# Kernel optimization log

Measured on AMD Instinct MI355X. Metric: run time of the kernel, lower is better.

Reference implementation:

```python
import jax, jax.numpy as jnp
import numpy as np
import math

B, T, C, H = 4, 2048, 1024, 4
D = C // H
SCALE = 1.0 / math.sqrt(D)
EPS = 1e-5

def _cln(x, w, b):
    # channel-first LayerNorm over C of (B, C, T)
    mu = jnp.mean(x, axis=1, keepdims=True)
    r = x - mu
    s = jnp.mean(r * r, axis=1, keepdims=True)
    return r / jnp.sqrt(s + EPS) * w + b

def _dwconv(x, w, b=None):
    # depthwise conv1d: x (B, C, T), w (C, 1, 3), stride 1, pad 1
    y = jax.lax.conv_general_dilated(x, w, (1,), [(1, 1)], dimension_numbers=('NCH', 'OIH', 'NCH'), feature_group_count=x.shape[1])
    if b is not None:
        y = y + b[None, :, None]
    return y

def _conv1x1(x, w, b):
    # pointwise conv: x (B, C, T), w (Cout, Cin), b (Cout,)
    return jnp.einsum('oc,bct->bot', w, x) + b[None, :, None]

def _forward(x, mask, norm1_w, norm1_b, qconv_w, kconv_w, vconv_w, qnorm_w, qnorm_b, knorm_w, knorm_b, vnorm_w, vnorm_b, q1_w, q1_b, k1_w, k1_b, v1_w, v1_b, proj_w, proj_b, norm2_w, norm2_b, lin1_w, lin1_b, tc_w, tc_b, lin2_w, lin2_b):
    xc = jnp.swapaxes(x, 1, 2)                      # (B, C, T)
    h = _cln(xc, norm1_w, norm1_b)
    mf = mask.astype(x.dtype)                       # (B, 1, T); stride 1 -> interpolate is identity
    q = _conv1x1(_cln(_dwconv(h, qconv_w) * mf, qnorm_w, qnorm_b), q1_w, q1_b)
    k = _conv1x1(_cln(_dwconv(h, kconv_w) * mf, knorm_w, knorm_b), k1_w, k1_b)
    v = _conv1x1(_cln(_dwconv(h, vconv_w) * mf, vnorm_w, vnorm_b), v1_w, v1_b)
    # (B, H, T, D)
    q = jnp.swapaxes(q.reshape(B, H, D, T), 2, 3)
    k = jnp.swapaxes(k.reshape(B, H, D, T), 2, 3)
    v = jnp.swapaxes(v.reshape(B, H, D, T), 2, 3)
    att = jnp.einsum('bhqd,bhkd->bhqk', q * SCALE, k)
    att = jnp.where(mask[:, :, None, :], att, -jnp.inf)
    att = jax.nn.softmax(att, axis=-1)
    out = jnp.einsum('bhqk,bhkd->bhqd', att, v * mf[:, :, :, None])
    out = jnp.swapaxes(out, 2, 3).reshape(B, C, T)
    out = _conv1x1(out, proj_w, proj_b) * mf        # qx_mask == mask for stride 1
    x = x + jnp.swapaxes(out, 1, 2)                 # residual, (B, T, C)
    # Local_cnn branch
    h2 = jnp.swapaxes(_cln(jnp.swapaxes(x, 1, 2), norm2_w, norm2_b), 1, 2)  # (B, T, C)
    y = h2 @ lin1_w.T + lin1_b
    y = jnp.swapaxes(_dwconv(jnp.swapaxes(y, 1, 2), tc_w, tc_b), 1, 2)
    y = jax.nn.gelu(y, approximate=False)
    y = y @ lin2_w.T + lin2_b
    return x + y

def setup_inputs():
    key = jax.random.key(0)
    ks = jax.random.split(key, 16)
    f32 = jnp.float32
    x = jax.random.normal(ks[0], (B, T, C), dtype=f32)
    lengths = jax.random.randint(ks[1], (B,), T // 2, T + 1)
    mask = jnp.arange(T)[None, None, :] < lengths[:, None, None]  # (B, 1, T) bool
    dw_std = math.sqrt(2.0 / 3.0)
    px_std = math.sqrt(2.0 / C)
    d = dict(x=x, mask=mask)
    d['norm1_w'] = jnp.ones((1, C, 1), f32); d['norm1_b'] = jnp.zeros((1, C, 1), f32)
    d['qconv_w'] = jax.random.normal(ks[2], (C, 1, 3), dtype=f32) * dw_std
    d['kconv_w'] = jax.random.normal(ks[3], (C, 1, 3), dtype=f32) * dw_std
    d['vconv_w'] = jax.random.normal(ks[4], (C, 1, 3), dtype=f32) * dw_std
    for nm in ['qnorm', 'knorm', 'vnorm']:
        d[nm + '_w'] = jnp.ones((1, C, 1), f32); d[nm + '_b'] = jnp.zeros((1, C, 1), f32)
    d['q1_w'] = jax.random.normal(ks[5], (C, C), dtype=f32) * px_std; d['q1_b'] = jnp.zeros((C,), f32)
    d['k1_w'] = jax.random.normal(ks[6], (C, C), dtype=f32) * px_std; d['k1_b'] = jnp.zeros((C,), f32)
    d['v1_w'] = jax.random.normal(ks[7], (C, C), dtype=f32) * px_std; d['v1_b'] = jnp.zeros((C,), f32)
    d['proj_w'] = jax.random.normal(ks[8], (C, C), dtype=f32) * px_std; d['proj_b'] = jnp.zeros((C,), f32)
    d['norm2_w'] = jnp.ones((1, C, 1), f32); d['norm2_b'] = jnp.zeros((1, C, 1), f32)
    d['lin1_w'] = jax.random.normal(ks[9], (C, C), dtype=f32) * 0.02; d['lin1_b'] = jnp.zeros((C,), f32)
    d['tc_w'] = jax.random.normal(ks[10], (C, 1, 3), dtype=f32) * dw_std; d['tc_b'] = jnp.zeros((C,), f32)
    d['lin2_w'] = jax.random.normal(ks[11], (C, C), dtype=f32) * 0.02; d['lin2_b'] = jnp.zeros((C,), f32)
    return d

def reference(x, mask, norm1_w, norm1_b, qconv_w, kconv_w, vconv_w, qnorm_w, qnorm_b, knorm_w, knorm_b, vnorm_w, vnorm_b, q1_w, q1_b, k1_w, k1_b, v1_w, v1_b, proj_w, proj_b, norm2_w, norm2_b, lin1_w, lin1_b, tc_w, tc_b, lin2_w, lin2_b):
    return _forward(x, mask, norm1_w, norm1_b, qconv_w, kconv_w, vconv_w, qnorm_w, qnorm_b, knorm_w, knorm_b, vnorm_w, vnorm_b, q1_w, q1_b, k1_w, k1_b, v1_w, v1_b, proj_w, proj_b, norm2_w, norm2_b, lin1_w, lin1_b, tc_w, tc_b, lin2_w, lin2_b)
```

## Files before the change

kernel.cpp:

```cpp
#include <hip/hip_runtime.h>

#define BB 4
#define TT 2048
#define CC 1024
#define HH 4
#define DD 256
#define MM (BB*TT)

#define EPSV 1e-5f
#define NEGBIG (-1e30f)
#define SCALEV 0.0625f

typedef unsigned short u16;
typedef unsigned int   u32;
typedef __bf16 bf16x8 __attribute__((ext_vector_type(8)));
typedef float  f32x4  __attribute__((ext_vector_type(4)));

typedef u32 __attribute__((address_space(1))) gu32;
typedef u32 __attribute__((address_space(3))) lu32;

__device__ __forceinline__ u16 f2bf(float f){
  u32 u = __builtin_bit_cast(u32, f);
  u32 r = (u + 0x7fffu + ((u >> 16) & 1u)) >> 16;
  return (u16)r;
}
__device__ __forceinline__ float bf2f(u16 h){
  u32 u = ((u32)h) << 16;
  return __builtin_bit_cast(float, u);
}
__device__ __forceinline__ void gload_lds16(const u16* g, u16* l){
  __builtin_amdgcn_global_load_lds((const gu32*)g, (lu32*)l, 16, 0, 0);
}
__device__ __forceinline__ u32 cvtpk_bf16(float lo, float hi){
  u32 r;
  asm("v_cvt_pk_bf16_f32 %0, %1, %2" : "=v"(r) : "v"(lo), "v"(hi));
  return r;
}

__global__ __launch_bounds__(256) void conv_w_kernel(
    const float* __restrict__ w0, const float* __restrict__ w1, const float* __restrict__ w2,
    const float* __restrict__ w3, const float* __restrict__ w4, const float* __restrict__ w5,
    u16* __restrict__ o0, u16* __restrict__ o1, u16* __restrict__ o2,
    u16* __restrict__ o3, u16* __restrict__ o4, u16* __restrict__ o5){
  const int i = (blockIdx.x * 256 + threadIdx.x) * 4;
  const float* wsrc[6] = {w0,w1,w2,w3,w4,w5};
  u16* odst[6] = {o0,o1,o2,o3,o4,o5};
#pragma unroll
  for (int k = 0; k < 6; ++k){
    float4 v = *(const float4*)(wsrc[k] + i);
    ushort4 p; p.x=f2bf(v.x); p.y=f2bf(v.y); p.z=f2bf(v.z); p.w=f2bf(v.w);
    *(ushort4*)(odst[k] + i) = p;
  }
}

template<int OUTBF>
__global__ __launch_bounds__(256) void ln_rows(const float* __restrict__ x,
    const float* __restrict__ g, const float* __restrict__ be, void* __restrict__ out){
  const int row = blockIdx.x, tid = threadIdx.x;
  const float4 v = ((const float4*)(x + (size_t)row * CC))[tid];
  float s  = v.x + v.y + v.z + v.w;
  float ss = v.x*v.x + v.y*v.y + v.z*v.z + v.w*v.w;
  __shared__ float sb[8];
#pragma unroll
  for (int o = 1; o < 64; o <<= 1){ s += __shfl_xor(s, o); ss += __shfl_xor(ss, o); }
  const int wid = tid >> 6, lane = tid & 63;
  if (lane == 0){ sb[wid] = s; sb[4 + wid] = ss; }
  __syncthreads();
  s  = sb[0] + sb[1] + sb[2] + sb[3];
  ss = sb[4] + sb[5] + sb[6] + sb[7];
  const float mu = s * (1.0f / CC);
  const float rstd = rsqrtf(ss * (1.0f / CC) - mu * mu + EPSV);
  const float4 gg = ((const float4*)g)[tid];
  const float4 bb = ((const float4*)be)[tid];
  const float r0 = (v.x - mu) * rstd * gg.x + bb.x;
  const float r1 = (v.y - mu) * rstd * gg.y + bb.y;
  const float r2 = (v.z - mu) * rstd * gg.z + bb.z;
  const float r3 = (v.w - mu) * rstd * gg.w + bb.w;
  if (OUTBF){
    ushort4 p; p.x=f2bf(r0); p.y=f2bf(r1); p.z=f2bf(r2); p.w=f2bf(r3);
    *(ushort4*)((u16*)out + (size_t)row * CC + tid * 4) = p;
  } else {
    ((float4*)((float*)out + (size_t)row * CC))[tid] = make_float4(r0, r1, r2, r3);
  }
}

__global__ __launch_bounds__(256) void qkv_pre(const float* __restrict__ h,
    const int* __restrict__ mask,
    const float* __restrict__ qw, const float* __restrict__ kw, const float* __restrict__ vw,
    const float* __restrict__ qg, const float* __restrict__ qb2,
    const float* __restrict__ kg, const float* __restrict__ kb2,
    const float* __restrict__ vg, const float* __restrict__ vb2,
    u16* __restrict__ qn, u16* __restrict__ kn, u16* __restrict__ vn){
  const int row = blockIdx.x, tid = threadIdx.x;
  const int t = row & (TT - 1);
  const float mf = mask[row] ? 1.f : 0.f;
  const float4 z4 = make_float4(0.f, 0.f, 0.f, 0.f);
  const float4 x0 = ((const float4*)(h + (size_t)row * CC))[tid];
  const float4 xm = (t > 0)      ? ((const float4*)(h + (size_t)(row - 1) * CC))[tid] : z4;
  const float4 xp = (t < TT - 1) ? ((const float4*)(h + (size_t)(row + 1) * CC))[tid] : z4;
  const int c = tid * 4;
  const float am[4] = {xm.x, xm.y, xm.z, xm.w};
  const float a0[4] = {x0.x, x0.y, x0.z, x0.w};
  const float ap[4] = {xp.x, xp.y, xp.z, xp.w};
  float yq[4], yk[4], yv[4];
  float sq=0.f, ssq=0.f, sk=0.f, ssk=0.f, sv=0.f, ssv=0.f;
#pragma unroll
  for (int i = 0; i < 4; ++i){
    const float* qwp = qw + (c + i) * 3;
    const float* kwp = kw + (c + i) * 3;
    const float* vwp = vw + (c + i) * 3;
    const float q_ = (am[i]*qwp[0] + a0[i]*qwp[1] + ap[i]*qwp[2]) * mf;
    const float k_ = (am[i]*kwp[0] + a0[i]*kwp[1] + ap[i]*kwp[2]) * mf;
    const float v_ = (am[i]*vwp[0] + a0[i]*vwp[1] + ap[i]*vwp[2]) * mf;
    yq[i]=q_; yk[i]=k_; yv[i]=v_;
    sq+=q_; ssq+=q_*q_; sk+=k_; ssk+=k_*k_; sv+=v_; ssv+=v_*v_;
  }
  __shared__ float sb[24];
#pragma unroll
  for (int o = 1; o < 64; o <<= 1){
    sq += __shfl_xor(sq, o); ssq += __shfl_xor(ssq, o);
    sk += __shfl_xor(sk, o); ssk += __shfl_xor(ssk, o);
    sv += __shfl_xor(sv, o); ssv += __shfl_xor(ssv, o);
  }
  const int wid = tid >> 6, lane = tid & 63;
  if (lane == 0){
    sb[wid]=sq; sb[4+wid]=ssq; sb[8+wid]=sk; sb[12+wid]=ssk; sb[16+wid]=sv; sb[20+wid]=ssv;
  }
  __syncthreads();
  sq  = sb[0]+sb[1]+sb[2]+sb[3];    ssq = sb[4]+sb[5]+sb[6]+sb[7];
  sk  = sb[8]+sb[9]+sb[10]+sb[11];  ssk = sb[12]+sb[13]+sb[14]+sb[15];
  sv  = sb[16]+sb[17]+sb[18]+sb[19];ssv = sb[20]+sb[21]+sb[22]+sb[23];
  {
    const float mu = sq * (1.f/CC), rstd = rsqrtf(ssq*(1.f/CC) - mu*mu + EPSV);
    ushort4 p;
    p.x = f2bf((yq[0]-mu)*rstd*qg[c+0] + qb2[c+0]);
    p.y = f2bf((yq[1]-mu)*rstd*qg[c+1] + qb2[c+1]);
    p.z = f2bf((yq[2]-mu)*rstd*qg[c+2] + qb2[c+2]);
    p.w = f2bf((yq[3]-mu)*rstd*qg[c+3] + qb2[c+3]);
    *(ushort4*)(qn + (size_t)row * CC + c) = p;
  }
  {
    const float mu = sk * (1.f/CC), rstd = rsqrtf(ssk*(1.f/CC) - mu*mu + EPSV);
    ushort4 p;
    p.x = f2bf((yk[0]-mu)*rstd*kg[c+0] + kb2[c+0]);
    p.y = f2bf((yk[1]-mu)*rstd*kg[c+1] + kb2[c+1]);
    p.z = f2bf((yk[2]-mu)*rstd*kg[c+2] + kb2[c+2]);
    p.w = f2bf((yk[3]-mu)*rstd*kg[c+3] + kb2[c+3]);
    *(ushort4*)(kn + (size_t)row * CC + c) = p;
  }
  {
    const float mu = sv * (1.f/CC), rstd = rsqrtf(ssv*(1.f/CC) - mu*mu + EPSV);
    ushort4 p;
    p.x = f2bf((yv[0]-mu)*rstd*vg[c+0] + vb2[c+0]);
    p.y = f2bf((yv[1]-mu)*rstd*vg[c+1] + vb2[c+1]);
    p.z = f2bf((yv[2]-mu)*rstd*vg[c+2] + vb2[c+2]);
    p.w = f2bf((yv[3]-mu)*rstd*vg[c+3] + vb2[c+3]);
    *(ushort4*)(vn + (size_t)row * CC + c) = p;
  }
}

__device__ __forceinline__ void gemm_core(const u16* __restrict__ A, const u16* __restrict__ Bw,
    u16* As, u16* Bs, f32x4 acc[4][4], int bm, int bn, int tid){
  const int lane = tid & 63, wid = tid >> 6;
  const int wr = wid >> 1, wc = wid & 1;
  const int la = lane & 15, lg = lane >> 4;
  const int srow = tid >> 3;
  const int schunk = (tid & 7) ^ (srow & 7);
  const u16* gA = A  + (size_t)(bm * 128 + srow) * CC + schunk * 8;
  const u16* gB = Bw + (size_t)(bn * 128 + srow) * CC + schunk * 8;
  u16* dA = As + tid * 8;
  u16* dB = Bs + tid * 8;
  const int swz = (la & 7) << 4;
  for (int kt = 0; kt < CC / 64; ++kt){
#pragma unroll
    for (int i = 0; i < 4; ++i){
      gload_lds16(gA + (size_t)(i * 32) * CC + kt * 64, dA + i * 2048);
      gload_lds16(gB + (size_t)(i * 32) * CC + kt * 64, dB + i * 2048);
    }
    __syncthreads();
#pragma unroll
    for (int kk = 0; kk < 2; ++kk){
      bf16x8 af[4], bf[4];
      const int co = (kk * 64 + lg * 16) ^ swz;
#pragma unroll
      for (int mi = 0; mi < 4; ++mi)
        af[mi] = *(const bf16x8*)((const char*)As + (wr * 64 + mi * 16 + la) * 128 + co);
#pragma unroll
      for (int ni = 0; ni < 4; ++ni)
        bf[ni] = *(const bf16x8*)((const char*)Bs + (wc * 64 + ni * 16 + la) * 128 + co);
#pragma unroll
      for (int mi = 0; mi < 4; ++mi)
#pragma unroll
        for (int ni = 0; ni < 4; ++ni)
          acc[mi][ni] = __builtin_amdgcn_mfma_f32_16x16x32_bf16(af[mi], bf[ni], acc[mi][ni], 0, 0, 0);
    }
    __syncthreads();
  }
}

template<int MODE>
__global__ __launch_bounds__(256) void gemm_bt(
    const u16* __restrict__ A, const u16* __restrict__ Bw,
    const float* __restrict__ bias, void* __restrict__ out,
    const float* __restrict__ resid, const int* __restrict__ mask){
  __shared__ __align__(16) u16 As[128 * 64];
  __shared__ __align__(16) u16 Bs[128 * 64];
  const int tid = threadIdx.x, lane = tid & 63, wid = tid >> 6;
  const int wr = wid >> 1, wc = wid & 1;
  const int bm = blockIdx.x, bn = blockIdx.y;
  f32x4 acc[4][4];
#pragma unroll
  for (int i = 0; i < 4; ++i)
#pragma unroll
    for (int j = 0; j < 4; ++j) acc[i][j] = (f32x4){0.f, 0.f, 0.f, 0.f};
  gemm_core(A, Bw, As, Bs, acc, bm, bn, tid);
  const int la = lane & 15, lg = lane >> 4;
#pragma unroll
  for (int mi = 0; mi < 4; ++mi){
    const int mb = bm * 128 + wr * 64 + mi * 16 + lg * 4;
#pragma unroll
    for (int ni = 0; ni < 4; ++ni){
      const int n = bn * 128 + wc * 64 + ni * 16 + la;
      const float bz = bias[n];
      if (MODE == 0){
        u16* o = (u16*)out;
#pragma unroll
        for (int j = 0; j < 4; ++j) o[(size_t)(mb + j) * CC + n] = f2bf(acc[mi][ni][j] + bz);
      } else if (MODE == 1){
        float* o = (float*)out;
#pragma unroll
        for (int j = 0; j < 4; ++j){
          const int m = mb + j;
          const float mf = mask[m] ? 1.f : 0.f;
          o[(size_t)m * CC + n] = (acc[mi][ni][j] + bz) * mf + resid[(size_t)m * CC + n];
        }
      } else {
        float* o = (float*)out;
#pragma unroll
        for (int j = 0; j < 4; ++j){
          const int m = mb + j;
          o[(size_t)m * CC + n] = acc[mi][ni][j] + bz + resid[(size_t)m * CC + n];
        }
      }
    }
  }
}

__global__ __launch_bounds__(256) void gemm_qkv(
    const u16* __restrict__ qn, const u16* __restrict__ kn, const u16* __restrict__ vn,
    const u16* __restrict__ wq, const u16* __restrict__ wk, const u16* __restrict__ wv,
    const float* __restrict__ qb, const float* __restrict__ kb, const float* __restrict__ vb,
    u16* __restrict__ Qb, u16* __restrict__ Kb, u16* __restrict__ Vtb){
  __shared__ __align__(16) u16 As[128 * 64];
  __shared__ __align__(16) u16 Bs[128 * 64];
  const int z = blockIdx.z;
  const u16* A  = (z == 0) ? qn : (z == 1) ? kn : vn;
  const u16* Bw = (z == 0) ? wq : (z == 1) ? wk : wv;
  const float* bias = (z == 0) ? qb : (z == 1) ? kb : vb;
  const int tid = threadIdx.x, lane = tid & 63, wid = tid >> 6;
  const int wr = wid >> 1, wc = wid & 1;
  const int bm = blockIdx.x, bn = blockIdx.y;
  f32x4 acc[4][4];
#pragma unroll
  for (int i = 0; i < 4; ++i)
#pragma unroll
    for (int j = 0; j < 4; ++j) acc[i][j] = (f32x4){0.f, 0.f, 0.f, 0.f};
  gemm_core(A, Bw, As, Bs, acc, bm, bn, tid);
  const int la = lane & 15, lg = lane >> 4;
#pragma unroll
  for (int mi = 0; mi < 4; ++mi){
    const int mb = bm * 128 + wr * 64 + mi * 16 + lg * 4;
#pragma unroll
    for (int ni = 0; ni < 4; ++ni){
      const int n = bn * 128 + wc * 64 + ni * 16 + la;
      const float bz = bias[n];
      if (z < 2){
        u16* o = z ? Kb : Qb;
#pragma unroll
        for (int j = 0; j < 4; ++j) o[(size_t)(mb + j) * CC + n] = f2bf(acc[mi][ni][j] + bz);
      } else {
        const int bq = mb >> 11, tq = mb & (TT - 1);
        const int hq = n >> 8, dq = n & 255;
        ushort4 p;
        p.x = f2bf(acc[mi][ni][0] + bz); p.y = f2bf(acc[mi][ni][1] + bz);
        p.z = f2bf(acc[mi][ni][2] + bz); p.w = f2bf(acc[mi][ni][3] + bz);
        *(ushort4*)&Vtb[(size_t)((bq * HH + hq) * DD + dq) * TT + tq] = p;
      }
    }
  }
}

__global__ __launch_bounds__(256, 3) void flash_attn(
    const u16* __restrict__ Q, const u16* __restrict__ Kg,
    const u16* __restrict__ Vt, const int* __restrict__ mask,
    u16* __restrict__ Oa){
  __shared__ __align__(16) u16 Ks[32 * 256];
  __shared__ __align__(16) u16 Vs[256 * 32];
  __shared__ __align__(16) u16 Ps[4][16 * 32];
  const int Dn = blockIdx.x;
  const int xcd = Dn & 7, idx = Dn >> 3;
  const int bh = xcd * 2 + (idx >> 5), qt = idx & 31;
  const int b = bh >> 2, h2 = bh & 3;
  const int tid = threadIdx.x, lane = tid & 63, wid = tid >> 6;
  const int la = lane & 15, lg = lane >> 4;

  const int* mrow = mask + b * TT;
  int len = 1024;
  {
    unsigned long long bal = __ballot(mrow[1024 + lane * 16] != 0);
    int ones = __popcll(bal);
    if (ones > 0){
      int lo = 1024 + (ones - 1) * 16;
      unsigned long long bal2 = __ballot(mrow[lo + la] != 0);
      len = lo + __popcll(bal2 & 0xFFFFull);
    }
  }
  const int nkt = (len + 31) >> 5;

  bf16x8 qf[8];
  const u16* qrow = Q + (size_t)(b * TT + qt * 64 + wid * 16 + la) * CC + h2 * DD + lg * 8;
#pragma unroll
  for (int kd = 0; kd < 8; ++kd) qf[kd] = *(const bf16x8*)(qrow + kd * 32);

  f32x4 oacc[16];
#pragma unroll
  for (int i = 0; i < 16; ++i) oacc[i] = (f32x4){0.f, 0.f, 0.f, 0.f};
  float mrun = NEGBIG, lrun = 0.f;

  const int krow = tid >> 5;
  const int kc = (tid & 31) ^ (krow & 7);
  const u16* ksrc = Kg + (size_t)(b * TT + krow) * CC + h2 * DD + kc * 8;
  const int vc = (tid & 3) ^ ((tid >> 3) & 3);
  const u16* vsrcb = Vt + (size_t)(bh * DD + (tid >> 2)) * TT + vc * 8;

#define STAGE_K(KT) { _Pragma("unroll") \
  for (int i = 0; i < 4; ++i) \
    gload_lds16(ksrc + (size_t)((KT) * 32 + i * 8) * CC, Ks + i * 2048 + tid * 8); }
#define STAGE_V(KT) { _Pragma("unroll") \
  for (int i = 0; i < 4; ++i) \
    gload_lds16(vsrcb + (size_t)(i * 64) * TT + (KT) * 32, Vs + i * 2048 + tid * 8); }

  STAGE_K(0); STAGE_V(0);
  __syncthreads();

  const char* KsB = (const char*)Ks;
  const char* VsB = (const char*)Vs;
  char* PsB = (char*)&Ps[wid][0];
  const int swk = (la & 7) << 4;
  const int swv = (la >> 1) & 3;
  const float sc2 = SCALEV * 1.44269504f;

  for (int kt = 0; kt < nkt; ++kt){
    f32x4 sfr[2];
#pragma unroll
    for (int fn = 0; fn < 2; ++fn){
      f32x4 s = (f32x4){0.f, 0.f, 0.f, 0.f};
      const int rk = fn * 16 + la;
#pragma unroll
      for (int kd = 0; kd < 8; ++kd){
        bf16x8 kf = *(const bf16x8*)(KsB + rk * 512 + ((kd * 64 + lg * 16) ^ swk));
        s = __builtin_amdgcn_mfma_f32_16x16x32_bf16(kf, qf[kd], s, 0, 0, 0);
      }
      sfr[fn] = s;
    }
    if (kt * 32 + 32 <= len){
      sfr[0] *= sc2; sfr[1] *= sc2;
    } else {
      const int kb = kt * 32 + lg * 4;
#pragma unroll
      for (int fn = 0; fn < 2; ++fn)
#pragma unroll
        for (int j = 0; j < 4; ++j)
          sfr[fn][j] = (kb + fn * 16 + j < len) ? sfr[fn][j] * sc2 : NEGBIG;
    }
    float tm = fmaxf(fmaxf(fmaxf(sfr[0][0], sfr[0][1]), fmaxf(sfr[0][2], sfr[0][3])),
                     fmaxf(fmaxf(sfr[1][0], sfr[1][1]), fmaxf(sfr[1][2], sfr[1][3])));
    tm = fmaxf(tm, __shfl_xor(tm, 16));
    tm = fmaxf(tm, __shfl_xor(tm, 32));
    if (!__all(tm <= mrun + 12.0f)){
      const float mn = fmaxf(mrun, tm);
      const float al = __builtin_exp2f(mrun - mn);
      mrun = mn; lrun *= al;
#pragma unroll
      for (int i = 0; i < 16; ++i) oacc[i] *= al;
    }
    float p0 = __builtin_exp2f(sfr[0][0] - mrun), p1 = __builtin_exp2f(sfr[0][1] - mrun);
    float p2 = __builtin_exp2f(sfr[0][2] - mrun), p3 = __builtin_exp2f(sfr[0][3] - mrun);
    float p4 = __builtin_exp2f(sfr[1][0] - mrun), p5 = __builtin_exp2f(sfr[1][1] - mrun);
    float p6 = __builtin_exp2f(sfr[1][2] - mrun), p7 = __builtin_exp2f(sfr[1][3] - mrun);
    float ts = ((p0 + p1) + (p2 + p3)) + ((p4 + p5) + (p6 + p7));
    ts += __shfl_xor(ts, 16);
    ts += __shfl_xor(ts, 32);
    lrun += ts;
    {
      uint2 w0; w0.x = cvtpk_bf16(p0, p1); w0.y = cvtpk_bf16(p2, p3);
      uint2 w1; w1.x = cvtpk_bf16(p4, p5); w1.y = cvtpk_bf16(p6, p7);
      char* pr = PsB + la * 64 + ((lg & 1) << 3);
      *(uint2*)(pr + ((((lg >> 1)    ) ^ swv) << 4)) = w0;
      *(uint2*)(pr + (((2 + (lg >> 1)) ^ swv) << 4)) = w1;
    }
    __syncthreads();
    if (kt + 1 < nkt) STAGE_K(kt + 1);
    bf16x8 pf = *(const bf16x8*)(PsB + la * 64 + ((lg ^ swv) << 4));
#pragma unroll
    for (int mi = 0; mi < 16; ++mi){
      bf16x8 vf = *(const bf16x8*)(VsB + (mi * 16 + la) * 64 + ((lg ^ swv) << 4));
      oacc[mi] = __builtin_amdgcn_mfma_f32_16x16x32_bf16(vf, pf, oacc[mi], 0, 0, 0);
    }
    __syncthreads();
    if (kt + 1 < nkt) STAGE_V(kt + 1);
  }
  const float inv = 1.f / lrun;
  u16* orow = Oa + (size_t)(b * TT + qt * 64 + wid * 16 + la) * CC + h2 * DD + lg * 4;
#pragma unroll
  for (int mi = 0; mi < 16; ++mi){
    ushort4 p;
    p.x = f2bf(oacc[mi][0] * inv); p.y = f2bf(oacc[mi][1] * inv);
    p.z = f2bf(oacc[mi][2] * inv); p.w = f2bf(oacc[mi][3] * inv);
    *(ushort4*)(orow + mi * 16) = p;
  }
#undef STAGE_K
#undef STAGE_V
}

__global__ __launch_bounds__(256) void tc_gelu(const u16* __restrict__ y2,
    const float* __restrict__ w, const float* __restrict__ bias, u16* __restrict__ y3){
  const int row = blockIdx.x, tid = threadIdx.x;
  const int t = row & (TT - 1);
  const int c = tid * 4;
  ushort4 z4; z4.x = z4.y = z4.z = z4.w = 0;
  const ushort4 u0 = *(const ushort4*)(y2 + (size_t)row * CC + c);
  const ushort4 um = (t > 0)      ? *(const ushort4*)(y2 + (size_t)(row - 1) * CC + c) : z4;
  const ushort4 up = (t < TT - 1) ? *(const ushort4*)(y2 + (size_t)(row + 1) * CC + c) : z4;
  const float am[4] = {bf2f(um.x), bf2f(um.y), bf2f(um.z), bf2f(um.w)};
  const float a0[4] = {bf2f(u0.x), bf2f(u0.y), bf2f(u0.z), bf2f(u0.w)};
  const float ap[4] = {bf2f(up.x), bf2f(up.y), bf2f(up.z), bf2f(up.w)};
  u16 pv[4];
#pragma unroll
  for (int i = 0; i < 4; ++i){
    const float* wp = w + (c + i) * 3;
    const float yv = am[i] * wp[0] + a0[i] * wp[1] + ap[i] * wp[2] + bias[c + i];
    const float ge = 0.5f * yv * (1.f + erff(yv * 0.7071067811865475f));
    pv[i] = f2bf(ge);
  }
  ushort4 p; p.x = pv[0]; p.y = pv[1]; p.z = pv[2]; p.w = pv[3];
  *(ushort4*)(y3 + (size_t)row * CC + c) = p;
}

extern "C" void kernel_launch(void* const* d_in, const int* in_sizes, int n_in,
                              void* d_out, int out_size, void* d_ws, size_t ws_size,
                              hipStream_t stream){
  const float* x     = (const float*)d_in[0];
  const int*   mask  = (const int*)d_in[1];
  const float* n1g   = (const float*)d_in[2];
  const float* n1b   = (const float*)d_in[3];
  const float* qconv = (const float*)d_in[4];
  const float* kconv = (const float*)d_in[5];
  const float* vconv = (const float*)d_in[6];
  const float* qg    = (const float*)d_in[7];
  const float* qbe   = (const float*)d_in[8];
  const float* kg    = (const float*)d_in[9];
  const float* kbe   = (const float*)d_in[10];
  const float* vg    = (const float*)d_in[11];
  const float* vbe   = (const float*)d_in[12];
  const float* q1w   = (const float*)d_in[13];
  const float* q1b   = (const float*)d_in[14];
  const float* k1w   = (const float*)d_in[15];
  const float* k1b   = (const float*)d_in[16];
  const float* v1w   = (const float*)d_in[17];
  const float* v1b   = (const float*)d_in[18];
  const float* pw    = (const float*)d_in[19];
  const float* pb    = (const float*)d_in[20];
  const float* n2g   = (const float*)d_in[21];
  const float* n2b   = (const float*)d_in[22];
  const float* l1w   = (const float*)d_in[23];
  const float* l1b   = (const float*)d_in[24];
  const float* tcw   = (const float*)d_in[25];
  const float* tcb   = (const float*)d_in[26];
  const float* l2w   = (const float*)d_in[27];
  const float* l2b   = (const float*)d_in[28];
  (void)in_sizes; (void)n_in; (void)out_size; (void)ws_size;

  char* ws = (char*)d_ws;
  const size_t MB = (size_t)1 << 20;
  u16* wq  = (u16*)(ws + 0 * MB);
  u16* wk  = (u16*)(ws + 2 * MB);
  u16* wv  = (u16*)(ws + 4 * MB);
  u16* wp2 = (u16*)(ws + 6 * MB);
  u16* wl1 = (u16*)(ws + 8 * MB);
  u16* wl2 = (u16*)(ws + 10 * MB);
  float* hbuf = (float*)(ws + 12 * MB);
  float* x2   = hbuf;
  u16* qn  = (u16*)(ws + 44 * MB);
  u16* kn  = (u16*)(ws + 60 * MB);
  u16* vn  = (u16*)(ws + 76 * MB);
  u16* Qb  = (u16*)(ws + 92 * MB);
  u16* Kb  = (u16*)(ws + 108 * MB);
  u16* Vtb = (u16*)(ws + 124 * MB);
  u16* AO  = qn;
  u16* y1  = kn;
  u16* y2  = vn;
  u16* y3  = Qb;

  conv_w_kernel<<<1024, 256, 0, stream>>>(q1w, k1w, v1w, pw, l1w, l2w, wq, wk, wv, wp2, wl1, wl2);
  ln_rows<0><<<MM, 256, 0, stream>>>(x, n1g, n1b, hbuf);
  qkv_pre<<<MM, 256, 0, stream>>>(hbuf, mask, qconv, kconv, vconv,
                                  qg, qbe, kg, kbe, vg, vbe, qn, kn, vn);
  gemm_qkv<<<dim3(64, 8, 3), 256, 0, stream>>>(qn, kn, vn, wq, wk, wv, q1b, k1b, v1b, Qb, Kb, Vtb);
  flash_attn<<<512, 256, 0, stream>>>(Qb, Kb, Vtb, mask, AO);
  gemm_bt<1><<<dim3(64, 8), 256, 0, stream>>>(AO, wp2, pb, x2, x, mask);
  ln_rows<1><<<MM, 256, 0, stream>>>(x2, n2g, n2b, y1);
  gemm_bt<0><<<dim3(64, 8), 256, 0, stream>>>(y1, wl1, l1b, y2, nullptr, nullptr);
  tc_gelu<<<MM, 256, 0, stream>>>(y2, tcw, tcb, y3);
  gemm_bt<2><<<dim3(64, 8), 256, 0, stream>>>(y3, wl2, l2b, (float*)d_out, x2, nullptr);
}
```

Measured before the change: 355.9 us.

## Split flash attention over key ranges with 32x32 MFMA and combine kernel

Each flash-attention block now handles 128 query rows and half of the key tiles (split-K). Partial outputs go to two buffers with per-row max and sum stats, and a new combine kernel merges them. The inner loop moves from 16x16x32 to 32x32x16 MFMA. P stays in registers via permlane32 swaps, which removes the LDS round-trip and the Ps buffer. This aims to cut LDS traffic and raise per-wave work. The cost is an extra kernel launch, extra global traffic for the partials, and bf16 rounding of unnormalised partial outputs, with launch bounds lowered to 2 blocks.

```diff
diff --git a/kernel.cpp b/kernel.cpp
--- a/kernel.cpp
+++ b/kernel.cpp
@@ -15,6 +15,7 @@
 typedef unsigned int   u32;
 typedef __bf16 bf16x8 __attribute__((ext_vector_type(8)));
 typedef float  f32x4  __attribute__((ext_vector_type(4)));
+typedef float  f32x16 __attribute__((ext_vector_type(16)));
 
 typedef u32 __attribute__((address_space(1))) gu32;
 typedef u32 __attribute__((address_space(3))) lu32;
@@ -290,19 +291,20 @@
   }
 }
 
-__global__ __launch_bounds__(256, 3) void flash_attn(
+__global__ __launch_bounds__(256, 2) void flash_attn(
     const u16* __restrict__ Q, const u16* __restrict__ Kg,
     const u16* __restrict__ Vt, const int* __restrict__ mask,
-    u16* __restrict__ Oa){
+    u16* __restrict__ Os0, u16* __restrict__ Os1, float2* __restrict__ stats){
   __shared__ __align__(16) u16 Ks[32 * 256];
   __shared__ __align__(16) u16 Vs[256 * 32];
-  __shared__ __align__(16) u16 Ps[4][16 * 32];
   const int Dn = blockIdx.x;
-  const int xcd = Dn & 7, idx = Dn >> 3;
-  const int bh = xcd * 2 + (idx >> 5), qt = idx & 31;
+  const int xcd = Dn & 7, rest = Dn >> 3;
+  const int bh = xcd * 2 + (rest >> 5);
+  const int sub = rest & 31;
+  const int qt = sub >> 1, sp = sub & 1;
   const int b = bh >> 2, h2 = bh & 3;
   const int tid = threadIdx.x, lane = tid & 63, wid = tid >> 6;
-  const int la = lane & 15, lg = lane >> 4;
+  const int l31 = lane & 31, hi = lane >> 5;
 
   const int* mrow = mask + b * TT;
   int len = 1024;
@@ -311,20 +313,25 @@
     int ones = __popcll(bal);
     if (ones > 0){
       int lo = 1024 + (ones - 1) * 16;
-      unsigned long long bal2 = __ballot(mrow[lo + la] != 0);
+      unsigned long long bal2 = __ballot(mrow[lo + (lane & 15)] != 0);
       len = lo + __popcll(bal2 & 0xFFFFull);
     }
   }
   const int nkt = (len + 31) >> 5;
-
-  bf16x8 qf[8];
-  const u16* qrow = Q + (size_t)(b * TT + qt * 64 + wid * 16 + la) * CC + h2 * DD + lg * 8;
-#pragma unroll
-  for (int kd = 0; kd < 8; ++kd) qf[kd] = *(const bf16x8*)(qrow + kd * 32);
-
-  f32x4 oacc[16];
-#pragma unroll
-  for (int i = 0; i < 16; ++i) oacc[i] = (f32x4){0.f, 0.f, 0.f, 0.f};
+  const int hk = (nkt + 1) >> 1;
+  const int t0 = sp ? hk : 0, t1 = sp ? nkt : hk;
+
+  const int q0 = qt * 128 + wid * 32;
+  bf16x8 qf[16];
+  const u16* qrow = Q + (size_t)(b * TT + q0 + l31) * CC + h2 * DD + hi * 8;
+#pragma unroll
+  for (int kd = 0; kd < 16; ++kd) qf[kd] = *(const bf16x8*)(qrow + kd * 16);
+
+  f32x16 acc[8];
+#pragma unroll
+  for (int i = 0; i < 8; ++i)
+#pragma unroll
+    for (int r = 0; r < 16; ++r) acc[i][r] = 0.f;
   float mrun = NEGBIG, lrun = 0.f;
 
   const int krow = tid >> 5;
@@ -340,87 +347,114 @@
   for (int i = 0; i < 4; ++i) \
     gload_lds16(vsrcb + (size_t)(i * 64) * TT + (KT) * 32, Vs + i * 2048 + tid * 8); }
 
-  STAGE_K(0); STAGE_V(0);
+  STAGE_K(t0); STAGE_V(t0);
   __syncthreads();
 
   const char* KsB = (const char*)Ks;
   const char* VsB = (const char*)Vs;
-  char* PsB = (char*)&Ps[wid][0];
-  const int swk = (la & 7) << 4;
-  const int swv = (la >> 1) & 3;
+  const int swk = (l31 & 7) << 4;
+  const int swv = ((l31 >> 1) & 3) << 4;
   const float sc2 = SCALEV * 1.44269504f;
 
-  for (int kt = 0; kt < nkt; ++kt){
-    f32x4 sfr[2];
-#pragma unroll
-    for (int fn = 0; fn < 2; ++fn){
-      f32x4 s = (f32x4){0.f, 0.f, 0.f, 0.f};
-      const int rk = fn * 16 + la;
-#pragma unroll
-      for (int kd = 0; kd < 8; ++kd){
-        bf16x8 kf = *(const bf16x8*)(KsB + rk * 512 + ((kd * 64 + lg * 16) ^ swk));
-        s = __builtin_amdgcn_mfma_f32_16x16x32_bf16(kf, qf[kd], s, 0, 0, 0);
+  for (int kt = t0; kt < t1; ++kt){
+    f32x16 s;
+#pragma unroll
+    for (int r = 0; r < 16; ++r) s[r] = 0.f;
+#pragma unroll
+    for (int kd = 0; kd < 16; ++kd){
+      bf16x8 kf = *(const bf16x8*)(KsB + l31 * 512 + ((kd * 32 + hi * 16) ^ swk));
+      s = __builtin_amdgcn_mfma_f32_32x32x16_bf16(kf, qf[kd], s, 0, 0, 0);
+    }
+    if (kt * 32 + 32 <= len){
+      s *= sc2;
+    } else {
+#pragma unroll
+      for (int r = 0; r < 16; ++r){
+        const int k = kt * 32 + (r & 3) + 8 * (r >> 2) + 4 * hi;
+        s[r] = (k < len) ? s[r] * sc2 : NEGBIG;
       }
-      sfr[fn] = s;
-    }
-    if (kt * 32 + 32 <= len){
-      sfr[0] *= sc2; sfr[1] *= sc2;
-    } else {
-      const int kb = kt * 32 + lg * 4;
-#pragma unroll
-      for (int fn = 0; fn < 2; ++fn)
-#pragma unroll
-        for (int j = 0; j < 4; ++j)
-          sfr[fn][j] = (kb + fn * 16 + j < len) ? sfr[fn][j] * sc2 : NEGBIG;
-    }
-    float tm = fmaxf(fmaxf(fmaxf(sfr[0][0], sfr[0][1]), fmaxf(sfr[0][2], sfr[0][3])),
-                     fmaxf(fmaxf(sfr[1][0], sfr[1][1]), fmaxf(sfr[1][2], sfr[1][3])));
-    tm = fmaxf(tm, __shfl_xor(tm, 16));
+    }
+    float tm = s[0];
+#pragma unroll
+    for (int r = 1; r < 16; ++r) tm = fmaxf(tm, s[r]);
     tm = fmaxf(tm, __shfl_xor(tm, 32));
     if (!__all(tm <= mrun + 12.0f)){
       const float mn = fmaxf(mrun, tm);
       const float al = __builtin_exp2f(mrun - mn);
       mrun = mn; lrun *= al;
 #pragma unroll
-      for (int i = 0; i < 16; ++i) oacc[i] *= al;
-    }
-    float p0 = __builtin_exp2f(sfr[0][0] - mrun), p1 = __builtin_exp2f(sfr[0][1] - mrun);
-    float p2 = __builtin_exp2f(sfr[0][2] - mrun), p3 = __builtin_exp2f(sfr[0][3] - mrun);
-    float p4 = __builtin_exp2f(sfr[1][0] - mrun), p5 = __builtin_exp2f(sfr[1][1] - mrun);
-    float p6 = __builtin_exp2f(sfr[1][2] - mrun), p7 = __builtin_exp2f(sfr[1][3] - mrun);
-    float ts = ((p0 + p1) + (p2 + p3)) + ((p4 + p5) + (p6 + p7));
-    ts += __shfl_xor(ts, 16);
+      for (int i = 0; i < 8; ++i) acc[i] *= al;
+    }
+    float p[16];
+    float ts = 0.f;
+#pragma unroll
+    for (int r = 0; r < 16; ++r){ p[r] = __builtin_exp2f(s[r] - mrun); ts += p[r]; }
     ts += __shfl_xor(ts, 32);
     lrun += ts;
-    {
-      uint2 w0; w0.x = cvtpk_bf16(p0, p1); w0.y = cvtpk_bf16(p2, p3);
-      uint2 w1; w1.x = cvtpk_bf16(p4, p5); w1.y = cvtpk_bf16(p6, p7);
-      char* pr = PsB + la * 64 + ((lg & 1) << 3);
-      *(uint2*)(pr + ((((lg >> 1)    ) ^ swv) << 4)) = w0;
-      *(uint2*)(pr + (((2 + (lg >> 1)) ^ swv) << 4)) = w1;
-    }
+    u32 w0 = cvtpk_bf16(p[0],  p[1]),  w1 = cvtpk_bf16(p[2],  p[3]);
+    u32 w2 = cvtpk_bf16(p[4],  p[5]),  w3 = cvtpk_bf16(p[6],  p[7]);
+    u32 w4 = cvtpk_bf16(p[8],  p[9]),  w5 = cvtpk_bf16(p[10], p[11]);
+    u32 w6 = cvtpk_bf16(p[12], p[13]), w7 = cvtpk_bf16(p[14], p[15]);
+    asm("v_permlane32_swap_b32 %0, %1" : "+v"(w0), "+v"(w2));
+    asm("v_permlane32_swap_b32 %0, %1" : "+v"(w1), "+v"(w3));
+    asm("v_permlane32_swap_b32 %0, %1" : "+v"(w4), "+v"(w6));
+    asm("v_permlane32_swap_b32 %0, %1" : "+v"(w5), "+v"(w7));
+    u32 pb0u[4] = {w0, w1, w2, w3};
+    u32 pb1u[4] = {w4, w5, w6, w7};
+    bf16x8 pb0 = __builtin_bit_cast(bf16x8, *(uint4*)pb0u);
+    bf16x8 pb1 = __builtin_bit_cast(bf16x8, *(uint4*)pb1u);
     __syncthreads();
-    if (kt + 1 < nkt) STAGE_K(kt + 1);
-    bf16x8 pf = *(const bf16x8*)(PsB + la * 64 + ((lg ^ swv) << 4));
-#pragma unroll
-    for (int mi = 0; mi < 16; ++mi){
-      bf16x8 vf = *(const bf16x8*)(VsB + (mi * 16 + la) * 64 + ((lg ^ swv) << 4));
-      oacc[mi] = __builtin_amdgcn_mfma_f32_16x16x32_bf16(vf, pf, oacc[mi], 0, 0, 0);
+    if (kt + 1 < t1) STAGE_K(kt + 1);
+#pragma unroll
+    for (int dt = 0; dt < 8; ++dt){
+      const char* vr = VsB + (dt * 32 + l31) * 64;
+      bf16x8 vf0 = *(const bf16x8*)(vr + ((hi * 16) ^ swv));
+      acc[dt] = __builtin_amdgcn_mfma_f32_32x32x16_bf16(vf0, pb0, acc[dt], 0, 0, 0);
+      bf16x8 vf1 = *(const bf16x8*)(vr + ((32 + hi * 16) ^ swv));
+      acc[dt] = __builtin_amdgcn_mfma_f32_32x32x16_bf16(vf1, pb1, acc[dt], 0, 0, 0);
     }
     __syncthreads();
-    if (kt + 1 < nkt) STAGE_V(kt + 1);
-  }
-  const float inv = 1.f / lrun;
-  u16* orow = Oa + (size_t)(b * TT + qt * 64 + wid * 16 + la) * CC + h2 * DD + lg * 4;
-#pragma unroll
-  for (int mi = 0; mi < 16; ++mi){
-    ushort4 p;
-    p.x = f2bf(oacc[mi][0] * inv); p.y = f2bf(oacc[mi][1] * inv);
-    p.z = f2bf(oacc[mi][2] * inv); p.w = f2bf(oacc[mi][3] * inv);
-    *(ushort4*)(orow + mi * 16) = p;
-  }
+    if (kt + 1 < t1) STAGE_V(kt + 1);
+  }
+  u16* Os = sp ? Os1 : Os0;
+  u16* orow = Os + (size_t)(b * TT + q0 + l31) * CC + h2 * DD + hi * 4;
+#pragma unroll
+  for (int dt = 0; dt < 8; ++dt)
+#pragma unroll
+    for (int rg = 0; rg < 4; ++rg){
+      ushort4 pk;
+      pk.x = f2bf(acc[dt][rg * 4 + 0]); pk.y = f2bf(acc[dt][rg * 4 + 1]);
+      pk.z = f2bf(acc[dt][rg * 4 + 2]); pk.w = f2bf(acc[dt][rg * 4 + 3]);
+      *(ushort4*)(orow + dt * 32 + rg * 8) = pk;
+    }
+  if (lane < 32)
+    stats[(size_t)((sp * 16 + bh) << 11) + q0 + l31] = make_float2(mrun, lrun);
 #undef STAGE_K
 #undef STAGE_V
+}
+
+__global__ __launch_bounds__(256) void attn_combine(
+    const u16* __restrict__ Os0, const u16* __restrict__ Os1,
+    const float2* __restrict__ stats, u16* __restrict__ AO){
+  const int row = blockIdx.x, tid = threadIdx.x;
+  const int b = row >> 11, q = row & (TT - 1);
+  const int h2 = tid >> 6;
+  const int bh = b * HH + h2;
+  const float2 sA = stats[(size_t)(bh << 11) + q];
+  const float2 sB = stats[(size_t)((16 + bh) << 11) + q];
+  const float m = fmaxf(sA.x, sB.x);
+  const float eA = __builtin_exp2f(sA.x - m), eB = __builtin_exp2f(sB.x - m);
+  const float l = sA.y * eA + sB.y * eB;
+  const float fA = eA / l, fB = eB / l;
+  const size_t off = (size_t)row * CC + tid * 4;
+  const ushort4 a = *(const ushort4*)(Os0 + off);
+  const ushort4 c = *(const ushort4*)(Os1 + off);
+  ushort4 o;
+  o.x = f2bf(bf2f(a.x) * fA + bf2f(c.x) * fB);
+  o.y = f2bf(bf2f(a.y) * fA + bf2f(c.y) * fB);
+  o.z = f2bf(bf2f(a.z) * fA + bf2f(c.z) * fB);
+  o.w = f2bf(bf2f(a.w) * fA + bf2f(c.w) * fB);
+  *(ushort4*)(AO + off) = o;
 }
 
 __global__ __launch_bounds__(256) void tc_gelu(const u16* __restrict__ y2,
@@ -497,7 +531,10 @@
   u16* Qb  = (u16*)(ws + 92 * MB);
   u16* Kb  = (u16*)(ws + 108 * MB);
   u16* Vtb = (u16*)(ws + 124 * MB);
+  float2* stats = (float2*)(ws + 140 * MB);
   u16* AO  = qn;
+  u16* Os0 = kn;
+  u16* Os1 = vn;
   u16* y1  = kn;
   u16* y2  = vn;
   u16* y3  = Qb;
@@ -507,7 +544,8 @@
   qkv_pre<<<MM, 256, 0, stream>>>(hbuf, mask, qconv, kconv, vconv,
                                   qg, qbe, kg, kbe, vg, vbe, qn, kn, vn);
   gemm_qkv<<<dim3(64, 8, 3), 256, 0, stream>>>(qn, kn, vn, wq, wk, wv, q1b, k1b, v1b, Qb, Kb, Vtb);
-  flash_attn<<<512, 256, 0, stream>>>(Qb, Kb, Vtb, mask, AO);
+  flash_attn<<<512, 256, 0, stream>>>(Qb, Kb, Vtb, mask, Os0, Os1, stats);
+  attn_combine<<<MM, 256, 0, stream>>>(Os0, Os1, stats, AO);
   gemm_bt<1><<<dim3(64, 8), 256, 0, stream>>>(AO, wp2, pb, x2, x, mask);
   ln_rows<1><<<MM, 256, 0, stream>>>(x2, n2g, n2b, y1);
   gemm_bt<0><<<dim3(64, 8), 256, 0, stream>>>(y1, wl1, l1b, y2, nullptr, nullptr);
```

Result: faster. 340.4 us (-4.3%).
